# Kernel optimization log

Hardware: AMD Instinct MI355X
Metric: run time of the kernel (lower is better)

Reference implementation:

```python
import jax, jax.numpy as jnp
import numpy as np
from jax import lax

Q_SCALE = 128.0  # Q1.7 fixed point: 1 sign bit, 7 fractional bits


def quant_comp(x):
    """Q1.7 quantize (floor, clamp to [-128,127]) then force LSB=1 in the
    8-bit two's-complement pattern (equivalent to integer bitwise-or 1),
    then dequantize. Matches quantize_and_compensate_activation."""
    q = jnp.clip(jnp.floor(x * Q_SCALE), -128.0, 127.0).astype(jnp.int32)
    q = jnp.bitwise_or(q, 1)  # set LSB; in-range stays in [-127, 127]
    return q.astype(jnp.float32) / Q_SCALE


def conv2d(x, w, b, pad):
    y = lax.conv_general_dilated(
        x, w, window_strides=(1, 1), padding=[(pad, pad), (pad, pad)],
        dimension_numbers=("NCHW", "OIHW", "NCHW"))
    return y + b[None, :, None, None]


def maxpool2(x):
    return lax.reduce_window(x, -jnp.inf, lax.max,
                             (1, 1, 2, 2), (1, 1, 2, 2), "VALID")


def setup_inputs() -> dict:
    key = jax.random.key(0)
    ks = jax.random.split(key, 12)
    B = 16384

    def u(k, shape, fan_in):
        bound = 1.0 / np.sqrt(fan_in)
        return jax.random.uniform(k, shape, jnp.float32, -bound, bound)

    return {
        "x": jax.random.normal(ks[0], (B, 1, 28, 28), jnp.float32),
        "conv1_w": u(ks[1], (6, 1, 5, 5), 1 * 25),
        "conv1_b": u(ks[2], (6,), 1 * 25),
        "conv2_w": u(ks[3], (16, 6, 5, 5), 6 * 25),
        "conv2_b": u(ks[4], (16,), 6 * 25),
        "fc1_w": u(ks[5], (120, 400), 400),
        "fc1_b": u(ks[6], (120,), 400),
        "fc2_w": u(ks[7], (84, 120), 120),
        "fc2_b": u(ks[8], (84,), 120),
        "fc3_w": u(ks[9], (10, 84), 84),
        "fc3_b": u(ks[10], (10,), 84),
        "quant_act": 1,
    }


def reference(x, conv1_w, conv1_b, conv2_w, conv2_b,
              fc1_w, fc1_b, fc2_w, fc2_b, fc3_w, fc3_b, quant_act):
    q = bool(quant_act)
    if q:
        x = quant_comp(x)
    x = maxpool2(jax.nn.relu(conv2d(x, conv1_w, conv1_b, pad=2)))  # [B,6,14,14]
    if q:
        x = quant_comp(x)
    x = maxpool2(jax.nn.relu(conv2d(x, conv2_w, conv2_b, pad=0)))  # [B,16,5,5]
    if q:
        x = quant_comp(x)
    x = x.reshape(x.shape[0], -1)  # [B,400]
    x = jax.nn.relu(x @ fc1_w.T + fc1_b)
    if q:
        x = quant_comp(x)
    # dropout is identity in eval mode
    x = jax.nn.relu(x @ fc2_w.T + fc2_b)
    if q:
        x = quant_comp(x)
    return x @ fc3_w.T + fc3_b  # [B,10]
```

## Files before the change

kernel.cpp:

```cpp
#include <hip/hip_runtime.h>

#define Q_INV (1.0f / 128.0f)

__device__ __forceinline__ float quant_comp_f(float v) {
    float f = floorf(v * 128.0f);
    f = fminf(fmaxf(f, -128.0f), 127.0f);
    int qi = (int)f;
    qi |= 1;
    return (float)qi * Q_INV;
}

__global__ __launch_bounds__(192) void conv_fused_kernel(
    const float* __restrict__ x,
    const float* __restrict__ c1w, const float* __restrict__ c1b,
    const float* __restrict__ c2w, const float* __restrict__ c2b,
    const int* __restrict__ qflag,
    float* __restrict__ act)
{
    __shared__ __align__(16) float shpool[3680];
    __shared__ float w1s[150];
    __shared__ float b1s[6];
    __shared__ float b2s[16];
    __shared__ __align__(16) float mid[6][14][20];

    float (*pin)[36] = reinterpret_cast<float(*)[36]>(shpool);

    const int t = threadIdx.x;
    const int img = blockIdx.x;
    const bool q = (qflag[0] != 0);

    for (int i = t; i < 1152; i += 192) shpool[i] = 0.0f;
    if (t < 150) w1s[t] = c1w[t];
    if (t < 6) b1s[t] = c1b[t];
    if (t < 16) b2s[t] = c2b[t];
    __syncthreads();

    const float* xi = x + (size_t)img * 784;
    for (int i = t; i < 784; i += 192) {
        float v = xi[i];
        if (q) v = quant_comp_f(v);
        pin[i / 28 + 2][i % 28 + 2] = v;
    }
    __syncthreads();

    float hmax1[14];
    if (t < 168) {
        const int c = t / 28, oh = t % 28;
        float acc[28];
        #pragma unroll
        for (int j = 0; j < 28; ++j) acc[j] = 0.0f;
        #pragma unroll
        for (int ky = 0; ky < 5; ++ky) {
            float rbf[32];
            const float4* pr = reinterpret_cast<const float4*>(&pin[oh + ky][0]);
            #pragma unroll
            for (int j = 0; j < 8; ++j) {
                float4 v = pr[j];
                rbf[4*j] = v.x; rbf[4*j+1] = v.y; rbf[4*j+2] = v.z; rbf[4*j+3] = v.w;
            }
            #pragma unroll
            for (int kx = 0; kx < 5; ++kx) {
                const float wv = w1s[c * 25 + ky * 5 + kx];
                #pragma unroll
                for (int ow = 0; ow < 28; ++ow)
                    acc[ow] = fmaf(rbf[ow + kx], wv, acc[ow]);
            }
        }
        const float bb = b1s[c];
        #pragma unroll
        for (int j = 0; j < 14; ++j) {
            float v0 = acc[2*j] + bb;
            float v1 = acc[2*j + 1] + bb;
            hmax1[j] = fmaxf(v0, v1);
        }
    }
    __syncthreads();
    if (t < 168) {
        const int c = t / 28, oh = t % 28;
        #pragma unroll
        for (int j = 0; j < 14; ++j) shpool[(c * 28 + oh) * 17 + j] = hmax1[j];
    }
    __syncthreads();
    if (t < 84) {
        const int c = t / 14, ph = t % 14;
        #pragma unroll
        for (int j = 0; j < 14; ++j) {
            float m = fmaxf(shpool[(c * 28 + 2 * ph) * 17 + j],
                            shpool[(c * 28 + 2 * ph + 1) * 17 + j]);
            m = fmaxf(m, 0.0f);
            if (q) m = quant_comp_f(m);
            mid[c][ph][j] = m;
        }
    }
    __syncthreads();

    {
        const float4* src = reinterpret_cast<const float4*>(c2w);
        float4* dst = reinterpret_cast<float4*>(shpool);
        for (int i = t; i < 600; i += 192) dst[i] = src[i];
    }
    __syncthreads();

    const float* w2s = shpool;
    float* rowmax2 = shpool + 2400;

    float hmax2[5];
    if (t < 160) {
        const int c = t / 10, oh = t % 10;
        float acc[10];
        #pragma unroll
        for (int j = 0; j < 10; ++j) acc[j] = 0.0f;
        #pragma unroll
        for (int ky = 0; ky < 5; ++ky) {
            float rb[6][16];
            #pragma unroll
            for (int ic = 0; ic < 6; ++ic) {
                const float4* mr = reinterpret_cast<const float4*>(&mid[ic][oh + ky][0]);
                #pragma unroll
                for (int j2 = 0; j2 < 4; ++j2) {
                    float4 v = mr[j2];
                    rb[ic][4*j2] = v.x; rb[ic][4*j2+1] = v.y;
                    rb[ic][4*j2+2] = v.z; rb[ic][4*j2+3] = v.w;
                }
            }
            #pragma unroll
            for (int kx = 0; kx < 5; ++kx) {
                #pragma unroll
                for (int ic = 0; ic < 6; ++ic) {
                    const float wv = w2s[(c * 6 + ic) * 25 + ky * 5 + kx];
                    #pragma unroll
                    for (int ow = 0; ow < 10; ++ow)
                        acc[ow] = fmaf(rb[ic][ow + kx], wv, acc[ow]);
                }
            }
        }
        const float bb = b2s[c];
        #pragma unroll
        for (int j = 0; j < 5; ++j) {
            float v0 = acc[2*j] + bb;
            float v1 = acc[2*j + 1] + bb;
            hmax2[j] = fmaxf(v0, v1);
        }
    }
    if (t < 160) {
        const int c = t / 10, oh = t % 10;
        #pragma unroll
        for (int j = 0; j < 5; ++j) rowmax2[(c * 10 + oh) * 8 + j] = hmax2[j];
    }
    __syncthreads();
    if (t < 80) {
        const int c = t / 5, ph = t % 5;
        float* ao = act + (size_t)img * 400;
        #pragma unroll
        for (int j = 0; j < 5; ++j) {
            float m = fmaxf(rowmax2[(c * 10 + 2 * ph) * 8 + j],
                            rowmax2[(c * 10 + 2 * ph + 1) * 8 + j]);
            m = fmaxf(m, 0.0f);
            if (q) m = quant_comp_f(m);
            ao[c * 25 + ph * 5 + j] = m;
        }
    }
}

__global__ __launch_bounds__(256) void fc_fused_kernel(
    const float* __restrict__ act,
    const float* __restrict__ w1, const float* __restrict__ b1,
    const float* __restrict__ w2, const float* __restrict__ b2,
    const float* __restrict__ w3, const float* __restrict__ b3,
    const int* __restrict__ qflag,
    float* __restrict__ out, int B)
{
    __shared__ __align__(16) float a0[16][404];
    __shared__ __align__(16) float a1[16][124];
    __shared__ __align__(16) float a2[16][88];

    const int t = threadIdx.x;
    const bool q = (qflag[0] != 0);
    const int base = blockIdx.x * 16;

    for (int i = t; i < 16 * 400; i += 256) {
        const int im = i / 400, k = i % 400;
        if (base + im < B) a0[im][k] = act[(size_t)(base + im) * 400 + k];
    }
    __syncthreads();

    const int im = t & 15;
    const int grp = t >> 4;

    for (int o = grp; o < 120; o += 16) {
        const float4* wr = reinterpret_cast<const float4*>(w1 + o * 400);
        const float4* ar = reinterpret_cast<const float4*>(&a0[im][0]);
        float acc = 0.0f;
        #pragma unroll 4
        for (int kk = 0; kk < 100; ++kk) {
            const float4 av = ar[kk];
            const float4 wv = wr[kk];
            acc = fmaf(av.x, wv.x, acc);
            acc = fmaf(av.y, wv.y, acc);
            acc = fmaf(av.z, wv.z, acc);
            acc = fmaf(av.w, wv.w, acc);
        }
        float v = acc + b1[o];
        v = fmaxf(v, 0.0f);
        a1[im][o] = q ? quant_comp_f(v) : v;
    }
    __syncthreads();

    for (int o = grp; o < 84; o += 16) {
        const float4* wr = reinterpret_cast<const float4*>(w2 + o * 120);
        const float4* ar = reinterpret_cast<const float4*>(&a1[im][0]);
        float acc = 0.0f;
        #pragma unroll 4
        for (int kk = 0; kk < 30; ++kk) {
            const float4 av = ar[kk];
            const float4 wv = wr[kk];
            acc = fmaf(av.x, wv.x, acc);
            acc = fmaf(av.y, wv.y, acc);
            acc = fmaf(av.z, wv.z, acc);
            acc = fmaf(av.w, wv.w, acc);
        }
        float v = acc + b2[o];
        v = fmaxf(v, 0.0f);
        a2[im][o] = q ? quant_comp_f(v) : v;
    }
    __syncthreads();

    for (int o = grp; o < 10; o += 16) {
        const float4* wr = reinterpret_cast<const float4*>(w3 + o * 84);
        const float4* ar = reinterpret_cast<const float4*>(&a2[im][0]);
        float acc = 0.0f;
        #pragma unroll
        for (int kk = 0; kk < 21; ++kk) {
            const float4 av = ar[kk];
            const float4 wv = wr[kk];
            acc = fmaf(av.x, wv.x, acc);
            acc = fmaf(av.y, wv.y, acc);
            acc = fmaf(av.z, wv.z, acc);
            acc = fmaf(av.w, wv.w, acc);
        }
        if (base + im < B) out[(size_t)(base + im) * 10 + o] = acc + b3[o];
    }
}

extern "C" void kernel_launch(void* const* d_in, const int* in_sizes, int n_in,
                              void* d_out, int out_size, void* d_ws, size_t ws_size,
                              hipStream_t stream) {
    const float* x     = (const float*)d_in[0];
    const float* c1w   = (const float*)d_in[1];
    const float* c1b   = (const float*)d_in[2];
    const float* c2w   = (const float*)d_in[3];
    const float* c2b   = (const float*)d_in[4];
    const float* fc1w  = (const float*)d_in[5];
    const float* fc1b  = (const float*)d_in[6];
    const float* fc2w  = (const float*)d_in[7];
    const float* fc2b  = (const float*)d_in[8];
    const float* fc3w  = (const float*)d_in[9];
    const float* fc3b  = (const float*)d_in[10];
    const int*   qflag = (const int*)d_in[11];
    float* out = (float*)d_out;

    const int B = in_sizes[0] / 784;
    float* act = (float*)d_ws;

    conv_fused_kernel<<<B, 192, 0, stream>>>(x, c1w, c1b, c2w, c2b, qflag, act);

    const int nblk = (B + 15) / 16;
    fc_fused_kernel<<<nblk, 256, 0, stream>>>(act, fc1w, fc1b, fc2w, fc2b,
                                              fc3w, fc3b, qflag, out, B);
}
```

Baseline: 332.5 us.

## Stage FC weights in shared memory by K-chunks and compute two outputs per thread

The FC kernel no longer reads weight rows straight from global memory for each output. It now streams 40-wide K-chunks of the fc1, fc2 and fc3 weights into a shared tile alongside matching activation chunks. Each thread keeps register accumulators for two adjacent outputs across chunks, so every activation float4 load feeds two FMAs. The aim is to cut uncoalesced global weight traffic and LDS loads per FMA, at the cost of many more __syncthreads calls per block.

```diff
diff --git a/kernel.cpp b/kernel.cpp
--- a/kernel.cpp
+++ b/kernel.cpp
@@ -170,75 +170,136 @@
     const int* __restrict__ qflag,
     float* __restrict__ out, int B)
 {
-    __shared__ __align__(16) float a0[16][404];
+    __shared__ __align__(16) float wt[120][44];
+    __shared__ __align__(16) float a0c[16][44];
     __shared__ __align__(16) float a1[16][124];
     __shared__ __align__(16) float a2[16][88];
 
     const int t = threadIdx.x;
     const bool q = (qflag[0] != 0);
     const int base = blockIdx.x * 16;
-
-    for (int i = t; i < 16 * 400; i += 256) {
-        const int im = i / 400, k = i % 400;
-        if (base + im < B) a0[im][k] = act[(size_t)(base + im) * 400 + k];
-    }
-    __syncthreads();
-
     const int im = t & 15;
     const int grp = t >> 4;
 
-    for (int o = grp; o < 120; o += 16) {
-        const float4* wr = reinterpret_cast<const float4*>(w1 + o * 400);
-        const float4* ar = reinterpret_cast<const float4*>(&a0[im][0]);
-        float acc = 0.0f;
-        #pragma unroll 4
-        for (int kk = 0; kk < 100; ++kk) {
-            const float4 av = ar[kk];
-            const float4 wv = wr[kk];
-            acc = fmaf(av.x, wv.x, acc);
-            acc = fmaf(av.y, wv.y, acc);
-            acc = fmaf(av.z, wv.z, acc);
-            acc = fmaf(av.w, wv.w, acc);
-        }
-        float v = acc + b1[o];
-        v = fmaxf(v, 0.0f);
-        a1[im][o] = q ? quant_comp_f(v) : v;
-    }
-    __syncthreads();
-
-    for (int o = grp; o < 84; o += 16) {
-        const float4* wr = reinterpret_cast<const float4*>(w2 + o * 120);
-        const float4* ar = reinterpret_cast<const float4*>(&a1[im][0]);
-        float acc = 0.0f;
-        #pragma unroll 4
-        for (int kk = 0; kk < 30; ++kk) {
-            const float4 av = ar[kk];
-            const float4 wv = wr[kk];
-            acc = fmaf(av.x, wv.x, acc);
-            acc = fmaf(av.y, wv.y, acc);
-            acc = fmaf(av.z, wv.z, acc);
-            acc = fmaf(av.w, wv.w, acc);
-        }
-        float v = acc + b2[o];
-        v = fmaxf(v, 0.0f);
-        a2[im][o] = q ? quant_comp_f(v) : v;
-    }
-    __syncthreads();
-
-    for (int o = grp; o < 10; o += 16) {
-        const float4* wr = reinterpret_cast<const float4*>(w3 + o * 84);
-        const float4* ar = reinterpret_cast<const float4*>(&a2[im][0]);
-        float acc = 0.0f;
-        #pragma unroll
-        for (int kk = 0; kk < 21; ++kk) {
-            const float4 av = ar[kk];
-            const float4 wv = wr[kk];
-            acc = fmaf(av.x, wv.x, acc);
-            acc = fmaf(av.y, wv.y, acc);
-            acc = fmaf(av.z, wv.z, acc);
-            acc = fmaf(av.w, wv.w, acc);
-        }
-        if (base + im < B) out[(size_t)(base + im) * 10 + o] = acc + b3[o];
+    float acc[8];
+    #pragma unroll
+    for (int j = 0; j < 8; ++j) acc[j] = 0.0f;
+
+    for (int ch = 0; ch < 10; ++ch) {
+        __syncthreads();
+        for (int i = t; i < 1200; i += 256) {
+            const int o = i / 10, s = i % 10;
+            *reinterpret_cast<float4*>(&wt[o][s * 4]) =
+                *reinterpret_cast<const float4*>(w1 + o * 400 + ch * 40 + s * 4);
+        }
+        for (int i = t; i < 640; i += 256) {
+            const int imm = i / 40, k = i % 40;
+            if (base + imm < B)
+                a0c[imm][k] = act[(size_t)(base + imm) * 400 + ch * 40 + k];
+        }
+        __syncthreads();
+        #pragma unroll
+        for (int r = 0; r < 4; ++r) {
+            const int o0 = r * 32 + 2 * grp;
+            if (o0 < 120) {
+                float s0 = acc[2*r], s1 = acc[2*r+1];
+                #pragma unroll
+                for (int kk = 0; kk < 10; ++kk) {
+                    const float4 av = *reinterpret_cast<const float4*>(&a0c[im][kk*4]);
+                    const float4 wa = *reinterpret_cast<const float4*>(&wt[o0][kk*4]);
+                    const float4 wb = *reinterpret_cast<const float4*>(&wt[o0+1][kk*4]);
+                    s0 = fmaf(av.x, wa.x, s0); s1 = fmaf(av.x, wb.x, s1);
+                    s0 = fmaf(av.y, wa.y, s0); s1 = fmaf(av.y, wb.y, s1);
+                    s0 = fmaf(av.z, wa.z, s0); s1 = fmaf(av.z, wb.z, s1);
+                    s0 = fmaf(av.w, wa.w, s0); s1 = fmaf(av.w, wb.w, s1);
+                }
+                acc[2*r] = s0; acc[2*r+1] = s1;
+            }
+        }
+    }
+    #pragma unroll
+    for (int r = 0; r < 4; ++r) {
+        const int o0 = r * 32 + 2 * grp;
+        if (o0 < 120) {
+            float v0 = acc[2*r] + b1[o0];
+            float v1 = acc[2*r+1] + b1[o0+1];
+            v0 = fmaxf(v0, 0.0f); v1 = fmaxf(v1, 0.0f);
+            a1[im][o0]   = q ? quant_comp_f(v0) : v0;
+            a1[im][o0+1] = q ? quant_comp_f(v1) : v1;
+        }
+    }
+
+    float bcc[6];
+    #pragma unroll
+    for (int j = 0; j < 6; ++j) bcc[j] = 0.0f;
+
+    for (int ch = 0; ch < 3; ++ch) {
+        __syncthreads();
+        for (int i = t; i < 840; i += 256) {
+            const int o = i / 10, s = i % 10;
+            *reinterpret_cast<float4*>(&wt[o][s * 4]) =
+                *reinterpret_cast<const float4*>(w2 + o * 120 + ch * 40 + s * 4);
+        }
+        __syncthreads();
+        #pragma unroll
+        for (int r = 0; r < 3; ++r) {
+            const int o0 = r * 32 + 2 * grp;
+            if (o0 < 84) {
+                float s0 = bcc[2*r], s1 = bcc[2*r+1];
+                #pragma unroll
+                for (int kk = 0; kk < 10; ++kk) {
+                    const float4 av = *reinterpret_cast<const float4*>(&a1[im][ch*40 + kk*4]);
+                    const float4 wa = *reinterpret_cast<const float4*>(&wt[o0][kk*4]);
+                    const float4 wb = *reinterpret_cast<const float4*>(&wt[o0+1][kk*4]);
+                    s0 = fmaf(av.x, wa.x, s0); s1 = fmaf(av.x, wb.x, s1);
+                    s0 = fmaf(av.y, wa.y, s0); s1 = fmaf(av.y, wb.y, s1);
+                    s0 = fmaf(av.z, wa.z, s0); s1 = fmaf(av.z, wb.z, s1);
+                    s0 = fmaf(av.w, wa.w, s0); s1 = fmaf(av.w, wb.w, s1);
+                }
+                bcc[2*r] = s0; bcc[2*r+1] = s1;
+            }
+        }
+    }
+    #pragma unroll
+    for (int r = 0; r < 3; ++r) {
+        const int o0 = r * 32 + 2 * grp;
+        if (o0 < 84) {
+            float v0 = bcc[2*r] + b2[o0];
+            float v1 = bcc[2*r+1] + b2[o0+1];
+            v0 = fmaxf(v0, 0.0f); v1 = fmaxf(v1, 0.0f);
+            a2[im][o0]   = q ? quant_comp_f(v0) : v0;
+            a2[im][o0+1] = q ? quant_comp_f(v1) : v1;
+        }
+    }
+
+    __syncthreads();
+    {
+        float* wtf = &wt[0][0];
+        for (int i = t; i < 210; i += 256)
+            reinterpret_cast<float4*>(wtf)[i] =
+                reinterpret_cast<const float4*>(w3)[i];
+    }
+    __syncthreads();
+    {
+        const int o0 = 2 * grp;
+        if (o0 < 10) {
+            const float* wtf = &wt[0][0];
+            float s0 = 0.0f, s1 = 0.0f;
+            #pragma unroll
+            for (int kk = 0; kk < 21; ++kk) {
+                const float4 av = *reinterpret_cast<const float4*>(&a2[im][kk*4]);
+                const float4 wa = *reinterpret_cast<const float4*>(&wtf[o0*84 + kk*4]);
+                const float4 wb = *reinterpret_cast<const float4*>(&wtf[(o0+1)*84 + kk*4]);
+                s0 = fmaf(av.x, wa.x, s0); s1 = fmaf(av.x, wb.x, s1);
+                s0 = fmaf(av.y, wa.y, s0); s1 = fmaf(av.y, wb.y, s1);
+                s0 = fmaf(av.z, wa.z, s0); s1 = fmaf(av.z, wb.z, s1);
+                s0 = fmaf(av.w, wa.w, s0); s1 = fmaf(av.w, wb.w, s1);
+            }
+            if (base + im < B) {
+                out[(size_t)(base + im) * 10 + o0]     = s0 + b3[o0];
+                out[(size_t)(base + im) * 10 + o0 + 1] = s1 + b3[o0 + 1];
+            }
+        }
     }
 }
 
```

After: 324.3 us. 1.03x faster.
